# Kernel optimization log

Measured on AMD Instinct MI355X. Metric: run time of the kernel, lower is better.

The kernel has to match this reference:

```python
import jax, jax.numpy as jnp
import numpy as np

D_EMBED, D_K, D_V = 1024, 64, 64
B, S = 4, 4096


def setup_inputs() -> dict:
    key = jax.random.key(0)
    k1, k2, k3, k4 = jax.random.split(key, 4)
    x = jax.random.normal(k1, (B, S, D_EMBED), dtype=jnp.float32)
    # nn.Linear(d_embed, d) stores weight as [d, d_embed]
    Wq = jax.random.normal(k2, (D_K, D_EMBED), dtype=jnp.float32) * (D_EMBED ** -0.5)
    Wk = jax.random.normal(k3, (D_K, D_EMBED), dtype=jnp.float32) * (D_EMBED ** -0.5)
    Wv = jax.random.normal(k4, (D_V, D_EMBED), dtype=jnp.float32) * (D_EMBED ** -0.5)
    return {"x": x, "Wq": Wq, "Wk": Wk, "Wv": Wv}


def reference(x, Wq, Wk, Wv):
    # self-attention: y = z = x
    key = jnp.einsum('bse,ke->bsk', x, Wk)
    query = jnp.einsum('bse,ke->bsk', x, Wq)
    value = jnp.einsum('bse,ve->bsv', x, Wv)
    d_k = key.shape[-1]
    weight = jnp.einsum('bqk,bsk->bqs', query, key) / (d_k ** 0.5)
    # Faithful to torch: tril then masked_fill(weight == 0, -inf)
    weight = jnp.tril(weight)
    weight = jnp.where(weight == 0, -jnp.inf, weight)
    weight = jax.nn.softmax(weight, axis=-1)
    return jnp.einsum('bqs,bsv->bqv', weight, value)
```

## Files before the change

kernel.cpp:

```cpp
#include <hip/hip_runtime.h>
#include <hip/hip_bf16.h>


typedef short s16x8 __attribute__((ext_vector_type(8)));
typedef float f32x4 __attribute__((ext_vector_type(4)));
typedef float f32x16 __attribute__((ext_vector_type(16)));
typedef unsigned u32x2 __attribute__((ext_vector_type(2)));
typedef union { unsigned u[4]; s16x8 v; } pfrag;

#define MFMA16(a, b, c) __builtin_amdgcn_mfma_f32_16x16x32_bf16(a, b, c, 0, 0, 0)
#define MFMA32(a, b, c) __builtin_amdgcn_mfma_f32_32x32x16_bf16(a, b, c, 0, 0, 0)

constexpr int SEQ = 4096;
constexpr int DE  = 1024;

__device__ __forceinline__ short f2bf(float f) {
    union { float f; unsigned u; } v; v.f = f;
    unsigned r = (v.u + 0x7FFFu + ((v.u >> 16) & 1u)) >> 16;
    return (short)r;
}
__device__ __forceinline__ unsigned fbits(float f) { union { float f; unsigned u; } v; v.f = f; return v.u; }
__device__ __forceinline__ float bitsf(unsigned u) { union { unsigned u; float f; } v; v.u = u; return v.f; }
__device__ __forceinline__ unsigned pk2(float a, float b) {
    return (fbits(b) & 0xFFFF0000u) | (fbits(a) >> 16);
}

#define GLDS(gp, lp)                                                          \
    __builtin_amdgcn_global_load_lds(                                         \
        (const __attribute__((address_space(1))) unsigned int*)(gp),          \
        (__attribute__((address_space(3))) unsigned int*)(lp), 16, 0, 0)

__global__ __launch_bounds__(256) void k_convw(const float* __restrict__ Wq,
                                               const float* __restrict__ Wk,
                                               const float* __restrict__ Wv,
                                               short* __restrict__ Wb) {
    int i = (blockIdx.x * 256 + threadIdx.x) * 4;
    if (i >= 192 * 1024) return;
    int n = i >> 10, k = i & 1023;
    const float* src; float sc;
    if (n < 64)       { src = Wq + n * 1024;         sc = 0.18033688011112042f; }
    else if (n < 128) { src = Wk + (n - 64) * 1024;  sc = 1.0f; }
    else              { src = Wv + (n - 128) * 1024; sc = 1.0f; }
    float4 v = *(const float4*)(src + k);
    short4 o;
    o.x = f2bf(v.x * sc); o.y = f2bf(v.y * sc);
    o.z = f2bf(v.z * sc); o.w = f2bf(v.w * sc);
    *(short4*)(Wb + i) = o;
}

__global__ __launch_bounds__(512) void k_proj(const float* __restrict__ x,
                                              const short* __restrict__ Wb,
                                              short* __restrict__ Qs,
                                              short* __restrict__ Ks,
                                              short* __restrict__ Vt) {
    __shared__ __align__(16) char lds[2][40960];
    const int tid  = threadIdx.x;
    const int lane = tid & 63;
    const int c = lane & 15, g = (lane >> 4) & 3;
    const int wv = tid >> 6;
    const int rg = wv & 3, nh = wv >> 2;
    const int n0 = nh * 96;
    const int m0 = blockIdx.x * 64;

    const int Ar  = tid >> 4;
    const int Acs = ((tid & 15) << 4) ^ ((Ar & 7) << 4);
    const char* aS0 = (const char*)x + (((size_t)(m0 + Ar)) << 12) + Acs;
    const char* aS1 = aS0 + ((size_t)32 << 12);
    const int Wr  = tid >> 3;
    const int Wcs = ((tid & 7) << 4) ^ ((Wr & 7) << 4);
    const char* wS0 = (const char*)Wb + (((size_t)Wr) << 11) + Wcs;
    const char* wS1 = wS0 + ((size_t)64 << 11);
    const char* wS2 = wS0 + ((size_t)128 << 11);

    char* db0 = &lds[0][0] + tid * 16;
    char* db1 = &lds[1][0] + tid * 16;

    const int arow = rg * 16 + c;
    const int swz  = (c & 7) << 4;
    const char* aR[2] = { &lds[0][0] + arow * 256, &lds[1][0] + arow * 256 };
    const char* wR[2][6];
#pragma unroll
    for (int nf = 0; nf < 6; nf++) {
        int wrow = n0 + nf * 16 + c;
        wR[0][nf] = &lds[0][0] + 16384 + wrow * 128;
        wR[1][nf] = &lds[1][0] + 16384 + wrow * 128;
    }

    f32x4 acc[6];
#pragma unroll
    for (int i = 0; i < 6; i++) acc[i] = (f32x4){0.f, 0.f, 0.f, 0.f};

#define PSTAGE(kk, db) {                                  \
        GLDS(aS0 + (kk) * 256, (db));                     \
        GLDS(aS1 + (kk) * 256, (db) + 8192);              \
        GLDS(wS0 + (kk) * 128, (db) + 16384);             \
        GLDS(wS1 + (kk) * 128, (db) + 24576);             \
        GLDS(wS2 + (kk) * 128, (db) + 32768); }

#define PCOMPUTE(bi) {                                                         \
        _Pragma("unroll")                                                      \
        for (int kc = 0; kc < 2; kc++) {                                       \
            float4 a0 = *(const float4*)(aR[bi] + ((kc*128 + g*32)      ^ swz)); \
            float4 a1 = *(const float4*)(aR[bi] + ((kc*128 + g*32 + 16) ^ swz)); \
            s16x8 a;                                                           \
            a[0]=f2bf(a0.x); a[1]=f2bf(a0.y); a[2]=f2bf(a0.z); a[3]=f2bf(a0.w); \
            a[4]=f2bf(a1.x); a[5]=f2bf(a1.y); a[6]=f2bf(a1.z); a[7]=f2bf(a1.w); \
            _Pragma("unroll")                                                  \
            for (int nf = 0; nf < 6; nf++) {                                   \
                s16x8 bfr = *(const s16x8*)(wR[bi][nf] + ((kc*64 + g*16) ^ swz)); \
                acc[nf] = MFMA16(a, bfr, acc[nf]);                             \
            }                                                                  \
        } }

    PSTAGE(0, db0);
    PSTAGE(1, db1);

    for (int kk = 0; kk < 15; kk++) {
        asm volatile("s_waitcnt vmcnt(5)" ::: "memory");
        __builtin_amdgcn_sched_barrier(0);
        __builtin_amdgcn_s_barrier();
        if (kk & 1) PCOMPUTE(1) else PCOMPUTE(0)
        asm volatile("s_waitcnt lgkmcnt(0)" ::: "memory");
        __builtin_amdgcn_sched_barrier(0);
        __builtin_amdgcn_s_barrier();
        if (kk < 14) { if (kk & 1) PSTAGE(kk + 2, db1) else PSTAGE(kk + 2, db0) }
    }
    asm volatile("s_waitcnt vmcnt(0)" ::: "memory");
    __builtin_amdgcn_sched_barrier(0);
    __builtin_amdgcn_s_barrier();
    PCOMPUTE(1)
#undef PSTAGE
#undef PCOMPUTE

#pragma unroll
    for (int nf = 0; nf < 6; nf++) {
        int col16 = n0 + nf * 16;
        if (col16 < 64) {
            int col = col16 + c;
#pragma unroll
            for (int r = 0; r < 4; r++)
                Qs[(size_t)(m0 + rg * 16 + g * 4 + r) * 64 + col] = f2bf(acc[nf][r]);
        } else if (col16 < 128) {
            int col = col16 - 64 + c;
#pragma unroll
            for (int r = 0; r < 4; r++)
                Ks[(size_t)(m0 + rg * 16 + g * 4 + r) * 64 + col] = f2bf(acc[nf][r]);
        } else {
            int d  = col16 - 128 + c;
            int mm = m0 + rg * 16 + g * 4;
            int bt = mm >> 12, s0 = mm & (SEQ - 1);
            short4 o;
            o.x = f2bf(acc[nf][0]); o.y = f2bf(acc[nf][1]);
            o.z = f2bf(acc[nf][2]); o.w = f2bf(acc[nf][3]);
            *(short4*)(Vt + ((size_t)(bt * 64 + d)) * SEQ + s0) = o;
        }
    }
}

#define SMTREE(sa, sb, m, ll, o0, o1) {                                        \
    float mx8[8];                                                              \
    _Pragma("unroll")                                                          \
    for (int i2 = 0; i2 < 8; i2++)                                             \
        mx8[i2] = fmaxf(fmaxf(sa[i2], sa[i2 + 8]), fmaxf(sb[i2], sb[i2 + 8])); \
    float tm_ = fmaxf(fmaxf(fmaxf(mx8[0], mx8[1]), fmaxf(mx8[2], mx8[3])),     \
                      fmaxf(fmaxf(mx8[4], mx8[5]), fmaxf(mx8[6], mx8[7])));    \
    u32x2 sw_ = __builtin_amdgcn_permlane32_swap(fbits(tm_), fbits(tm_), false, false); \
    tm_ = fmaxf(bitsf(sw_[0]), bitsf(sw_[1]));                                 \
    float mn_ = fmaxf(m, tm_);                                                 \
    float sc_ = __builtin_amdgcn_exp2f(m - mn_);                               \
    m = mn_;                                                                   \
    _Pragma("unroll")                                                          \
    for (int i2 = 0; i2 < 16; i2++) {                                          \
        sa[i2] = __builtin_amdgcn_exp2f(sa[i2] - mn_);                         \
        sb[i2] = __builtin_amdgcn_exp2f(sb[i2] - mn_);                         \
    }                                                                          \
    float s8_[8];                                                              \
    _Pragma("unroll")                                                          \
    for (int i2 = 0; i2 < 8; i2++)                                             \
        s8_[i2] = (sa[i2] + sa[i2 + 8]) + (sb[i2] + sb[i2 + 8]);               \
    float ss_ = ((s8_[0] + s8_[1]) + (s8_[2] + s8_[3]))                        \
              + ((s8_[4] + s8_[5]) + (s8_[6] + s8_[7]));                       \
    sw_ = __builtin_amdgcn_permlane32_swap(fbits(ss_), fbits(ss_), false, false); \
    ss_ = bitsf(sw_[0]) + bitsf(sw_[1]);                                       \
    ll = ll * sc_ + ss_;                                                       \
    o0 *= sc_; o1 *= sc_; }

#define PACKPH(sa, sb, u0, u1, u2, u3) {                                       \
    unsigned A0 = pk2(sa[0], sa[1]),   B0 = pk2(sa[2], sa[3]);                 \
    unsigned A1 = pk2(sa[4], sa[5]),   B1 = pk2(sa[6], sa[7]);                 \
    unsigned A2 = pk2(sa[8], sa[9]),   B2 = pk2(sa[10], sa[11]);               \
    unsigned A3 = pk2(sa[12], sa[13]), B3 = pk2(sa[14], sa[15]);               \
    u32x2 r0_ = __builtin_amdgcn_permlane32_swap(A0, A1, false, false);        \
    u32x2 r1_ = __builtin_amdgcn_permlane32_swap(B0, B1, false, false);        \
    u32x2 r2_ = __builtin_amdgcn_permlane32_swap(A2, A3, false, false);        \
    u32x2 r3_ = __builtin_amdgcn_permlane32_swap(B2, B3, false, false);        \
    u0.u[0] = r0_[0]; u0.u[1] = r1_[0]; u0.u[2] = r0_[1]; u0.u[3] = r1_[1];    \
    u1.u[0] = r2_[0]; u1.u[1] = r3_[0]; u1.u[2] = r2_[1]; u1.u[3] = r3_[1];    \
    A0 = pk2(sb[0], sb[1]);   B0 = pk2(sb[2], sb[3]);                          \
    A1 = pk2(sb[4], sb[5]);   B1 = pk2(sb[6], sb[7]);                          \
    A2 = pk2(sb[8], sb[9]);   B2 = pk2(sb[10], sb[11]);                        \
    A3 = pk2(sb[12], sb[13]); B3 = pk2(sb[14], sb[15]);                        \
    r0_ = __builtin_amdgcn_permlane32_swap(A0, A1, false, false);              \
    r1_ = __builtin_amdgcn_permlane32_swap(B0, B1, false, false);              \
    r2_ = __builtin_amdgcn_permlane32_swap(A2, A3, false, false);              \
    r3_ = __builtin_amdgcn_permlane32_swap(B2, B3, false, false);              \
    u2.u[0] = r0_[0]; u2.u[1] = r1_[0]; u2.u[2] = r0_[1]; u2.u[3] = r1_[1];    \
    u3.u[0] = r2_[0]; u3.u[1] = r3_[0]; u3.u[2] = r2_[1]; u3.u[3] = r3_[1]; }

#define PROCT(qf, q0t, endt, m, ll, o0, o1) {                                  \
    if (k0 < (endt)) {                                                         \
        f32x16 sa = {}, sb = {};                                               \
        _Pragma("unroll")                                                      \
        for (int dd = 0; dd < 4; dd++) {                                       \
            int ch = ((2 * dd + hi) ^ qs7) << 4;                               \
            s16x8 ka  = *(const s16x8*)(kl + q * 128 + ch);                    \
            s16x8 kb2 = *(const s16x8*)(kl + (32 + q) * 128 + ch);             \
            sa = MFMA32(ka,  qf[dd], sa);                                      \
            sb = MFMA32(kb2, qf[dd], sb);                                      \
        }                                                                      \
        if (k0 + 31 > (q0t)) {                                                 \
            _Pragma("unroll")                                                  \
            for (int rr = 0; rr < 16; rr++) {                                  \
                int kv = k0 + (rr & 3) + 8 * (rr >> 2) + 4 * hi;               \
                if (kv > (q0t) + q) sa[rr] = -3.0e38f;                         \
            }                                                                  \
        }                                                                      \
        if (k0 + 63 > (q0t)) {                                                 \
            _Pragma("unroll")                                                  \
            for (int rr = 0; rr < 16; rr++) {                                  \
                int kv = k0 + 32 + (rr & 3) + 8 * (rr >> 2) + 4 * hi;          \
                if (kv > (q0t) + q) sb[rr] = -3.0e38f;                         \
            }                                                                  \
        }                                                                      \
        SMTREE(sa, sb, m, ll, o0, o1);                                         \
        pfrag u0_, u1_, u2_, u3_;                                              \
        PACKPH(sa, sb, u0_, u1_, u2_, u3_);                                    \
        _Pragma("unroll")                                                      \
        for (int dd = 0; dd < 4; dd++) {                                       \
            int ch = ((2 * dd + hi) ^ qs7) << 4;                               \
            s16x8 va  = *(const s16x8*)(vl + q * 128 + ch);                    \
            s16x8 vb2 = *(const s16x8*)(vl + (32 + q) * 128 + ch);             \
            pfrag* uu = dd == 0 ? &u0_ : dd == 1 ? &u1_ : dd == 2 ? &u2_ : &u3_; \
            o0 = MFMA32(va,  uu->v, o0);                                       \
            o1 = MFMA32(vb2, uu->v, o1);                                       \
        }                                                                      \
    } }

__global__ __launch_bounds__(256, 2) void k_attn(const short* __restrict__ Qs,
                                                 const short* __restrict__ Ks,
                                                 const short* __restrict__ Vt,
                                                 float* __restrict__ pws) {
    __shared__ __align__(16) char smem[2][16384];

    int tid = threadIdx.x;
    int l = tid & 63, wv = tid >> 6;
    int q = l & 31, hi = l >> 5;

    int ub = blockIdx.x >> 2, bt = blockIdx.x & 3;
    int u = ub, J = 15, cs = 8;
    while (u >= cs) { u -= cs; --J; cs = (J + 2) >> 1; }
    int seg = u;
    int kb0 = seg << 9;
    int kend_t = min(J * 256 + 256, kb0 + 512);
    const int R = (kend_t - kb0) >> 6;
    const int q0A = J * 256 + wv * 32;
    const int q0B = q0A + 128;
    const int endA = q0A + 32, endB = q0B + 32;

    const short* Qb = Qs + (size_t)bt * SEQ * 64;
    const short* Kb = Ks + (size_t)bt * SEQ * 64;
    const short* Vb = Vt + (size_t)bt * 64 * SEQ;

    s16x8 qfA[4], qfB[4];
#pragma unroll
    for (int d = 0; d < 4; d++) {
        qfA[d] = *(const s16x8*)(Qb + (size_t)(q0A + q) * 64 + d * 16 + hi * 8);
        qfB[d] = *(const s16x8*)(Qb + (size_t)(q0B + q) * 64 + d * 16 + hi * 8);
    }

    const int row8 = l >> 3;
    const int scs  = (l & 7) ^ row8;

#define ASTAGE(kb, b) {                                                        \
        _Pragma("unroll")                                                      \
        for (int i = 0; i < 2; i++) {                                          \
            GLDS(Kb + (((size_t)((kb) + wv*16 + i*8 + row8)) << 6) + scs*8,    \
                 &smem[b][0] + (wv*16 + i*8)*128);                             \
            GLDS(Vb + (size_t)(wv*16 + i*8 + row8) * SEQ + (kb) + scs*8,       \
                 &smem[b][0] + 8192 + (wv*16 + i*8)*128); } }

    f32x16 oA0 = {}, oA1 = {}, oB0 = {}, oB1 = {};
    float mA = -1e30f, llA = 0.f, mB = -1e30f, llB = 0.f;
    const int qs7 = q & 7;

    ASTAGE(kb0, 0);
    if (R > 1) ASTAGE(kb0 + 64, 1);

    for (int r = 0; r < R; r++) {
        if (r == R - 1) asm volatile("s_waitcnt vmcnt(0)" ::: "memory");
        else            asm volatile("s_waitcnt vmcnt(4)" ::: "memory");
        __builtin_amdgcn_sched_barrier(0);
        __builtin_amdgcn_s_barrier();
        __builtin_amdgcn_sched_barrier(0);

        int k0 = kb0 + r * 64;
        const char* kl = &smem[r & 1][0];
        const char* vl = kl + 8192;

        if (k0 + 63 <= q0A) {
            s16x8 kf[8];
#pragma unroll
            for (int dd = 0; dd < 4; dd++) {
                int ch = ((2 * dd + hi) ^ qs7) << 4;
                kf[dd]     = *(const s16x8*)(kl + q * 128 + ch);
                kf[4 + dd] = *(const s16x8*)(kl + (32 + q) * 128 + ch);
            }
            f32x16 saA = {}, sbA = {}, saB = {}, sbB = {};
#pragma unroll
            for (int dd = 0; dd < 4; dd++) {
                saA = MFMA32(kf[dd],     qfA[dd], saA);
                sbA = MFMA32(kf[4 + dd], qfA[dd], sbA);
                saB = MFMA32(kf[dd],     qfB[dd], saB);
                sbB = MFMA32(kf[4 + dd], qfB[dd], sbB);
            }
            SMTREE(saA, sbA, mA, llA, oA0, oA1);
            pfrag uA0, uA1, uA2, uA3;
            PACKPH(saA, sbA, uA0, uA1, uA2, uA3);
            s16x8 vf[8];
#pragma unroll
            for (int dd = 0; dd < 4; dd++) {
                int ch = ((2 * dd + hi) ^ qs7) << 4;
                vf[dd]     = *(const s16x8*)(vl + q * 128 + ch);
                vf[4 + dd] = *(const s16x8*)(vl + (32 + q) * 128 + ch);
            }
            oA0 = MFMA32(vf[0], uA0.v, oA0);
            oA0 = MFMA32(vf[1], uA1.v, oA0);
            oA0 = MFMA32(vf[2], uA2.v, oA0);
            oA0 = MFMA32(vf[3], uA3.v, oA0);
            oA1 = MFMA32(vf[4], uA0.v, oA1);
            oA1 = MFMA32(vf[5], uA1.v, oA1);
            oA1 = MFMA32(vf[6], uA2.v, oA1);
            oA1 = MFMA32(vf[7], uA3.v, oA1);
            SMTREE(saB, sbB, mB, llB, oB0, oB1);
            pfrag uB0, uB1, uB2, uB3;
            PACKPH(saB, sbB, uB0, uB1, uB2, uB3);
            oB0 = MFMA32(vf[0], uB0.v, oB0);
            oB0 = MFMA32(vf[1], uB1.v, oB0);
            oB0 = MFMA32(vf[2], uB2.v, oB0);
            oB0 = MFMA32(vf[3], uB3.v, oB0);
            oB1 = MFMA32(vf[4], uB0.v, oB1);
            oB1 = MFMA32(vf[5], uB1.v, oB1);
            oB1 = MFMA32(vf[6], uB2.v, oB1);
            oB1 = MFMA32(vf[7], uB3.v, oB1);
        } else {
            PROCT(qfA, q0A, endA, mA, llA, oA0, oA1);
            PROCT(qfB, q0B, endB, mB, llB, oB0, oB1);
        }

        asm volatile("s_waitcnt lgkmcnt(0)" ::: "memory");
        __builtin_amdgcn_sched_barrier(0);
        __builtin_amdgcn_s_barrier();
        if (r + 2 < R) { if (r & 1) ASTAGE(kb0 + (r + 2) * 64, 1) else ASTAGE(kb0 + (r + 2) * 64, 0) }
    }
#undef ASTAGE

    {
        float* p = pws + ((size_t)(((bt * 16 + J) * 8 + wv) * 8 + seg)) * 2112;
#pragma unroll
        for (int rr = 0; rr < 16; rr++) {
            int dv = (rr & 3) + 8 * (rr >> 2) + 4 * hi;
            p[dv * 32 + q]        = oA0[rr];
            p[(dv + 32) * 32 + q] = oA1[rr];
        }
        if (hi == 0) { p[2048 + q] = mA; p[2080 + q] = llA; }
    }
    {
        float* p = pws + ((size_t)(((bt * 16 + J) * 8 + 4 + wv) * 8 + seg)) * 2112;
#pragma unroll
        for (int rr = 0; rr < 16; rr++) {
            int dv = (rr & 3) + 8 * (rr >> 2) + 4 * hi;
            p[dv * 32 + q]        = oB0[rr];
            p[(dv + 32) * 32 + q] = oB1[rr];
        }
        if (hi == 0) { p[2048 + q] = mB; p[2080 + q] = llB; }
    }
}

__global__ __launch_bounds__(256) void k_comb(const float* __restrict__ pws,
                                              float* __restrict__ out) {
    int b = blockIdx.x;
    int sub = b & 7, J = (b >> 3) & 15, bt = b >> 7;
    int qbase = J * 256 + (sub >> 2) * 128 + (sub & 3) * 32;
    int nseg = (qbase + 32 + 511) >> 9;

    int tid = threadIdx.x;
    int q = tid >> 3, dv0 = (tid & 7) * 8;
    const float* base = pws + (size_t)b * 8 * 2112;

    float ms[8], wsg[8];
    float M = -1e30f;
#pragma unroll
    for (int s = 0; s < 8; s++) {
        if (s < nseg) { ms[s] = base[s * 2112 + 2048 + q]; M = fmaxf(M, ms[s]); }
    }
    float L = 0.f;
#pragma unroll
    for (int s = 0; s < 8; s++) {
        if (s < nseg) {
            wsg[s] = __builtin_amdgcn_exp2f(ms[s] - M);
            L += wsg[s] * base[s * 2112 + 2080 + q];
        }
    }
    float inv = 1.0f / L;
    float res[8];
#pragma unroll
    for (int i = 0; i < 8; i++) res[i] = 0.f;
#pragma unroll
    for (int s = 0; s < 8; s++) {
        if (s < nseg) {
            const float* po = base + s * 2112;
#pragma unroll
            for (int i = 0; i < 8; i++) res[i] += wsg[s] * po[(dv0 + i) * 32 + q];
        }
    }
    float* op = out + ((size_t)bt * SEQ + qbase + q) * 64 + dv0;
    float4 f0 = {res[0] * inv, res[1] * inv, res[2] * inv, res[3] * inv};
    float4 f1 = {res[4] * inv, res[5] * inv, res[6] * inv, res[7] * inv};
    *(float4*)op = f0;
    *(float4*)(op + 4) = f1;
}

extern "C" void kernel_launch(void* const* d_in, const int* in_sizes, int n_in,
                              void* d_out, int out_size, void* d_ws, size_t ws_size,
                              hipStream_t stream) {
    const float* x  = (const float*)d_in[0];
    const float* Wq = (const float*)d_in[1];
    const float* Wk = (const float*)d_in[2];
    const float* Wv = (const float*)d_in[3];
    float* out = (float*)d_out;

    char* ws = (char*)d_ws;
    short* Wb = (short*)ws;
    short* Qs = (short*)(ws + 393216);
    short* Ks = (short*)(ws + 393216 + 2097152);
    short* Vt = (short*)(ws + 393216 + 2 * 2097152);
    float* pP = (float*)(ws + 6684672);

    k_convw<<<dim3(192), dim3(256), 0, stream>>>(Wq, Wk, Wv, Wb);
    k_proj <<<dim3(256), dim3(512), 0, stream>>>(x, Wb, Qs, Ks, Vt);
    k_attn <<<dim3(288), dim3(256), 0, stream>>>(Qs, Ks, Vt, pP);
    k_comb <<<dim3(512), dim3(256), 0, stream>>>(pP, out);
}
```

Baseline: 71.73 us.

## Split attention work into 128-row query tiles with one tile per wave

```diff
diff --git a/kernel.cpp b/kernel.cpp
--- a/kernel.cpp
+++ b/kernel.cpp
@@ -207,45 +207,6 @@
     u2.u[0] = r0_[0]; u2.u[1] = r1_[0]; u2.u[2] = r0_[1]; u2.u[3] = r1_[1];    \
     u3.u[0] = r2_[0]; u3.u[1] = r3_[0]; u3.u[2] = r2_[1]; u3.u[3] = r3_[1]; }
 
-#define PROCT(qf, q0t, endt, m, ll, o0, o1) {                                  \
-    if (k0 < (endt)) {                                                         \
-        f32x16 sa = {}, sb = {};                                               \
-        _Pragma("unroll")                                                      \
-        for (int dd = 0; dd < 4; dd++) {                                       \
-            int ch = ((2 * dd + hi) ^ qs7) << 4;                               \
-            s16x8 ka  = *(const s16x8*)(kl + q * 128 + ch);                    \
-            s16x8 kb2 = *(const s16x8*)(kl + (32 + q) * 128 + ch);             \
-            sa = MFMA32(ka,  qf[dd], sa);                                      \
-            sb = MFMA32(kb2, qf[dd], sb);                                      \
-        }                                                                      \
-        if (k0 + 31 > (q0t)) {                                                 \
-            _Pragma("unroll")                                                  \
-            for (int rr = 0; rr < 16; rr++) {                                  \
-                int kv = k0 + (rr & 3) + 8 * (rr >> 2) + 4 * hi;               \
-                if (kv > (q0t) + q) sa[rr] = -3.0e38f;                         \
-            }                                                                  \
-        }                                                                      \
-        if (k0 + 63 > (q0t)) {                                                 \
-            _Pragma("unroll")                                                  \
-            for (int rr = 0; rr < 16; rr++) {                                  \
-                int kv = k0 + 32 + (rr & 3) + 8 * (rr >> 2) + 4 * hi;          \
-                if (kv > (q0t) + q) sb[rr] = -3.0e38f;                         \
-            }                                                                  \
-        }                                                                      \
-        SMTREE(sa, sb, m, ll, o0, o1);                                         \
-        pfrag u0_, u1_, u2_, u3_;                                              \
-        PACKPH(sa, sb, u0_, u1_, u2_, u3_);                                    \
-        _Pragma("unroll")                                                      \
-        for (int dd = 0; dd < 4; dd++) {                                       \
-            int ch = ((2 * dd + hi) ^ qs7) << 4;                               \
-            s16x8 va  = *(const s16x8*)(vl + q * 128 + ch);                    \
-            s16x8 vb2 = *(const s16x8*)(vl + (32 + q) * 128 + ch);             \
-            pfrag* uu = dd == 0 ? &u0_ : dd == 1 ? &u1_ : dd == 2 ? &u2_ : &u3_; \
-            o0 = MFMA32(va,  uu->v, o0);                                       \
-            o1 = MFMA32(vb2, uu->v, o1);                                       \
-        }                                                                      \
-    } }
-
 __global__ __launch_bounds__(256, 2) void k_attn(const short* __restrict__ Qs,
                                                  const short* __restrict__ Ks,
                                                  const short* __restrict__ Vt,
@@ -257,26 +218,23 @@
     int q = l & 31, hi = l >> 5;
 
     int ub = blockIdx.x >> 2, bt = blockIdx.x & 3;
-    int u = ub, J = 15, cs = 8;
-    while (u >= cs) { u -= cs; --J; cs = (J + 2) >> 1; }
+    int u = ub, j = 31, cs = 8;
+    while (u >= cs) { u -= cs; --j; cs = (j + 4) >> 2; }
     int seg = u;
     int kb0 = seg << 9;
-    int kend_t = min(J * 256 + 256, kb0 + 512);
-    const int R = (kend_t - kb0) >> 6;
-    const int q0A = J * 256 + wv * 32;
-    const int q0B = q0A + 128;
-    const int endA = q0A + 32, endB = q0B + 32;
+    int kend_t = min(j * 128 + 128, kb0 + 512);
+    const int R = (kend_t - kb0 + 63) >> 6;
+    const int q0 = j * 128 + wv * 32;
+    const int mycend = q0 + 32;
 
     const short* Qb = Qs + (size_t)bt * SEQ * 64;
     const short* Kb = Ks + (size_t)bt * SEQ * 64;
     const short* Vb = Vt + (size_t)bt * 64 * SEQ;
 
-    s16x8 qfA[4], qfB[4];
-#pragma unroll
-    for (int d = 0; d < 4; d++) {
-        qfA[d] = *(const s16x8*)(Qb + (size_t)(q0A + q) * 64 + d * 16 + hi * 8);
-        qfB[d] = *(const s16x8*)(Qb + (size_t)(q0B + q) * 64 + d * 16 + hi * 8);
-    }
+    s16x8 qf[4];
+#pragma unroll
+    for (int d = 0; d < 4; d++)
+        qf[d] = *(const s16x8*)(Qb + (size_t)(q0 + q) * 64 + d * 16 + hi * 8);
 
     const int row8 = l >> 3;
     const int scs  = (l & 7) ^ row8;
@@ -289,8 +247,8 @@
             GLDS(Vb + (size_t)(wv*16 + i*8 + row8) * SEQ + (kb) + scs*8,       \
                  &smem[b][0] + 8192 + (wv*16 + i*8)*128); } }
 
-    f32x16 oA0 = {}, oA1 = {}, oB0 = {}, oB1 = {};
-    float mA = -1e30f, llA = 0.f, mB = -1e30f, llB = 0.f;
+    f32x16 o0 = {}, o1 = {};
+    float m = -1e30f, ll = 0.f;
     const int qs7 = q & 7;
 
     ASTAGE(kb0, 0);
@@ -301,101 +259,83 @@
         else            asm volatile("s_waitcnt vmcnt(4)" ::: "memory");
         __builtin_amdgcn_sched_barrier(0);
         __builtin_amdgcn_s_barrier();
-        __builtin_amdgcn_sched_barrier(0);
-
-        int k0 = kb0 + r * 64;
+
         const char* kl = &smem[r & 1][0];
         const char* vl = kl + 8192;
-
-        if (k0 + 63 <= q0A) {
-            s16x8 kf[8];
-#pragma unroll
-            for (int dd = 0; dd < 4; dd++) {
-                int ch = ((2 * dd + hi) ^ qs7) << 4;
-                kf[dd]     = *(const s16x8*)(kl + q * 128 + ch);
-                kf[4 + dd] = *(const s16x8*)(kl + (32 + q) * 128 + ch);
-            }
-            f32x16 saA = {}, sbA = {}, saB = {}, sbB = {};
-#pragma unroll
-            for (int dd = 0; dd < 4; dd++) {
-                saA = MFMA32(kf[dd],     qfA[dd], saA);
-                sbA = MFMA32(kf[4 + dd], qfA[dd], sbA);
-                saB = MFMA32(kf[dd],     qfB[dd], saB);
-                sbB = MFMA32(kf[4 + dd], qfB[dd], sbB);
-            }
-            SMTREE(saA, sbA, mA, llA, oA0, oA1);
-            pfrag uA0, uA1, uA2, uA3;
-            PACKPH(saA, sbA, uA0, uA1, uA2, uA3);
-            s16x8 vf[8];
-#pragma unroll
-            for (int dd = 0; dd < 4; dd++) {
-                int ch = ((2 * dd + hi) ^ qs7) << 4;
-                vf[dd]     = *(const s16x8*)(vl + q * 128 + ch);
-                vf[4 + dd] = *(const s16x8*)(vl + (32 + q) * 128 + ch);
-            }
-            oA0 = MFMA32(vf[0], uA0.v, oA0);
-            oA0 = MFMA32(vf[1], uA1.v, oA0);
-            oA0 = MFMA32(vf[2], uA2.v, oA0);
-            oA0 = MFMA32(vf[3], uA3.v, oA0);
-            oA1 = MFMA32(vf[4], uA0.v, oA1);
-            oA1 = MFMA32(vf[5], uA1.v, oA1);
-            oA1 = MFMA32(vf[6], uA2.v, oA1);
-            oA1 = MFMA32(vf[7], uA3.v, oA1);
-            SMTREE(saB, sbB, mB, llB, oB0, oB1);
-            pfrag uB0, uB1, uB2, uB3;
-            PACKPH(saB, sbB, uB0, uB1, uB2, uB3);
-            oB0 = MFMA32(vf[0], uB0.v, oB0);
-            oB0 = MFMA32(vf[1], uB1.v, oB0);
-            oB0 = MFMA32(vf[2], uB2.v, oB0);
-            oB0 = MFMA32(vf[3], uB3.v, oB0);
-            oB1 = MFMA32(vf[4], uB0.v, oB1);
-            oB1 = MFMA32(vf[5], uB1.v, oB1);
-            oB1 = MFMA32(vf[6], uB2.v, oB1);
-            oB1 = MFMA32(vf[7], uB3.v, oB1);
-        } else {
-            PROCT(qfA, q0A, endA, mA, llA, oA0, oA1);
-            PROCT(qfB, q0B, endB, mB, llB, oB0, oB1);
-        }
-
+        s16x8 kf[8], vf[8];
+#pragma unroll
+        for (int dd = 0; dd < 4; dd++) {
+            int ch = ((2 * dd + hi) ^ qs7) << 4;
+            kf[dd]     = *(const s16x8*)(kl + q * 128 + ch);
+            kf[4 + dd] = *(const s16x8*)(kl + (32 + q) * 128 + ch);
+            vf[dd]     = *(const s16x8*)(vl + q * 128 + ch);
+            vf[4 + dd] = *(const s16x8*)(vl + (32 + q) * 128 + ch);
+        }
         asm volatile("s_waitcnt lgkmcnt(0)" ::: "memory");
         __builtin_amdgcn_sched_barrier(0);
         __builtin_amdgcn_s_barrier();
         if (r + 2 < R) { if (r & 1) ASTAGE(kb0 + (r + 2) * 64, 1) else ASTAGE(kb0 + (r + 2) * 64, 0) }
+
+        int k0 = kb0 + r * 64;
+        if (k0 < mycend) {
+            f32x16 sa = {}, sb = {};
+            __builtin_amdgcn_s_setprio(1);
+#pragma unroll
+            for (int dd = 0; dd < 4; dd++) {
+                sa = MFMA32(kf[dd],     qf[dd], sa);
+                sb = MFMA32(kf[4 + dd], qf[dd], sb);
+            }
+            __builtin_amdgcn_s_setprio(0);
+            if (k0 + 31 > q0) {
+#pragma unroll
+                for (int rr = 0; rr < 16; rr++) {
+                    int kv = k0 + (rr & 3) + 8 * (rr >> 2) + 4 * hi;
+                    if (kv > q0 + q) sa[rr] = -3.0e38f;
+                }
+            }
+            if (k0 + 63 > q0) {
+#pragma unroll
+                for (int rr = 0; rr < 16; rr++) {
+                    int kv = k0 + 32 + (rr & 3) + 8 * (rr >> 2) + 4 * hi;
+                    if (kv > q0 + q) sb[rr] = -3.0e38f;
+                }
+            }
+            SMTREE(sa, sb, m, ll, o0, o1);
+            pfrag u0_, u1_, u2_, u3_;
+            PACKPH(sa, sb, u0_, u1_, u2_, u3_);
+            __builtin_amdgcn_s_setprio(1);
+            o0 = MFMA32(vf[0], u0_.v, o0);
+            o0 = MFMA32(vf[1], u1_.v, o0);
+            o0 = MFMA32(vf[2], u2_.v, o0);
+            o0 = MFMA32(vf[3], u3_.v, o0);
+            o1 = MFMA32(vf[4], u0_.v, o1);
+            o1 = MFMA32(vf[5], u1_.v, o1);
+            o1 = MFMA32(vf[6], u2_.v, o1);
+            o1 = MFMA32(vf[7], u3_.v, o1);
+            __builtin_amdgcn_s_setprio(0);
+        }
     }
 #undef ASTAGE
 
-    {
-        float* p = pws + ((size_t)(((bt * 16 + J) * 8 + wv) * 8 + seg)) * 2112;
-#pragma unroll
-        for (int rr = 0; rr < 16; rr++) {
-            int dv = (rr & 3) + 8 * (rr >> 2) + 4 * hi;
-            p[dv * 32 + q]        = oA0[rr];
-            p[(dv + 32) * 32 + q] = oA1[rr];
-        }
-        if (hi == 0) { p[2048 + q] = mA; p[2080 + q] = llA; }
-    }
-    {
-        float* p = pws + ((size_t)(((bt * 16 + J) * 8 + 4 + wv) * 8 + seg)) * 2112;
-#pragma unroll
-        for (int rr = 0; rr < 16; rr++) {
-            int dv = (rr & 3) + 8 * (rr >> 2) + 4 * hi;
-            p[dv * 32 + q]        = oB0[rr];
-            p[(dv + 32) * 32 + q] = oB1[rr];
-        }
-        if (hi == 0) { p[2048 + q] = mB; p[2080 + q] = llB; }
-    }
+    float* p = pws + ((((size_t)(bt * 32 + j) * 4 + wv) * 8 + seg)) * 2112;
+#pragma unroll
+    for (int rr = 0; rr < 16; rr++) {
+        int dv = (rr & 3) + 8 * (rr >> 2) + 4 * hi;
+        p[dv * 32 + q]        = o0[rr];
+        p[(dv + 32) * 32 + q] = o1[rr];
+    }
+    if (hi == 0) { p[2048 + q] = m; p[2080 + q] = ll; }
 }
 
 __global__ __launch_bounds__(256) void k_comb(const float* __restrict__ pws,
                                               float* __restrict__ out) {
     int b = blockIdx.x;
-    int sub = b & 7, J = (b >> 3) & 15, bt = b >> 7;
-    int qbase = J * 256 + (sub >> 2) * 128 + (sub & 3) * 32;
-    int nseg = (qbase + 32 + 511) >> 9;
+    int w = b & 3, j = (b >> 2) & 31, bt = b >> 7;
+    int nseg = (j + 4) >> 2;
 
     int tid = threadIdx.x;
     int q = tid >> 3, dv0 = (tid & 7) * 8;
-    const float* base = pws + (size_t)b * 8 * 2112;
+    const float* base = pws + ((size_t)(bt * 32 + j) * 4 + w) * 8 * 2112;
 
     float ms[8], wsg[8];
     float M = -1e30f;
@@ -423,7 +363,7 @@
             for (int i = 0; i < 8; i++) res[i] += wsg[s] * po[(dv0 + i) * 32 + q];
         }
     }
-    float* op = out + ((size_t)bt * SEQ + qbase + q) * 64 + dv0;
+    float* op = out + ((size_t)bt * SEQ + j * 128 + w * 32 + q) * 64 + dv0;
     float4 f0 = {res[0] * inv, res[1] * inv, res[2] * inv, res[3] * inv};
     float4 f1 = {res[4] * inv, res[5] * inv, res[6] * inv, res[7] * inv};
     *(float4*)op = f0;
@@ -448,6 +388,6 @@
 
     k_convw<<<dim3(192), dim3(256), 0, stream>>>(Wq, Wk, Wv, Wb);
     k_proj <<<dim3(256), dim3(512), 0, stream>>>(x, Wb, Qs, Ks, Vt);
-    k_attn <<<dim3(288), dim3(256), 0, stream>>>(Qs, Ks, Vt, pP);
+    k_attn <<<dim3(576), dim3(256), 0, stream>>>(Qs, Ks, Vt, pP);
     k_comb <<<dim3(512), dim3(256), 0, stream>>>(pP, out);
 }
```

Measured after the change: 68.43 us. 4.6% less time.
